# Kernel optimization log

Measured on AMD Instinct MI355X. Metric: run time of the kernel, lower is better.

The kernel has to match this reference:

```python
import jax, jax.numpy as jnp
import numpy as np

B, D, H, S = 32768, 512, 8, 3  # batch, stream_dim, heads, num_streams
DH = D // H
EPS = 1e-5


def setup_inputs() -> dict:
    key = jax.random.key(0)
    ks = jax.random.split(key, 16)
    sc = lambda fan_in: 1.0 / np.sqrt(fan_in)
    return {
        "kinematic_h": jax.random.normal(ks[0], (B, D), jnp.float32),
        "color_h": jax.random.normal(ks[1], (B, D), jnp.float32),
        "spinor_h": jax.random.normal(ks[2], (B, D), jnp.float32),
        # MultiheadAttention packed in-proj and out-proj
        "w_in": jax.random.normal(ks[3], (3 * D, D), jnp.float32) * sc(D),
        "b_in": jnp.zeros((3 * D,), jnp.float32),
        "w_out": jax.random.normal(ks[4], (D, D), jnp.float32) * sc(D),
        "b_out": jnp.zeros((D,), jnp.float32),
        # stream gate: Linear(3D -> 3) + softmax
        "w_gate": jax.random.normal(ks[5], (S, S * D), jnp.float32) * sc(S * D),
        "b_gate": jnp.zeros((S,), jnp.float32),
        # fusion MLP: Linear(3D -> 2D), SiLU, Linear(2D -> D)
        "w1": jax.random.normal(ks[6], (2 * D, S * D), jnp.float32) * sc(S * D),
        "b1": jnp.zeros((2 * D,), jnp.float32),
        "w2": jax.random.normal(ks[7], (D, 2 * D), jnp.float32) * sc(2 * D),
        "b2": jnp.zeros((D,), jnp.float32),
        # LayerNorm
        "gamma": jnp.ones((D,), jnp.float32),
        "beta": jnp.zeros((D,), jnp.float32),
    }


def reference(kinematic_h, color_h, spinor_h, w_in, b_in, w_out, b_out,
              w_gate, b_gate, w1, b1, w2, b2, gamma, beta):
    stacked = jnp.stack([kinematic_h, color_h, spinor_h], axis=1)  # [B,S,D]
    b = stacked.shape[0]
    # self-attention (Q=K=V=stacked), packed QKV projection
    qkv = stacked @ w_in.T + b_in  # [B,S,3D]
    q, k, v = jnp.split(qkv, 3, axis=-1)
    q = q.reshape(b, S, H, DH)
    k = k.reshape(b, S, H, DH)
    v = v.reshape(b, S, H, DH)
    scores = jnp.einsum("bqhd,bkhd->bhqk", q, k) / np.sqrt(DH)
    attn = jax.nn.softmax(scores, axis=-1)
    out = jnp.einsum("bhqk,bkhd->bqhd", attn, v).reshape(b, S, D)
    attn_out = stacked + (out @ w_out.T + b_out)  # residual, [B,S,D]
    # gating softmax over streams
    flat = attn_out.reshape(b, S * D)
    gates = jax.nn.softmax(flat @ w_gate.T + b_gate, axis=-1)[..., None]  # [B,S,1]
    gated = (attn_out * gates).reshape(b, S * D)
    # fusion MLP (dropout=eval no-op)
    h = jax.nn.silu(gated @ w1.T + b1)
    fused = h @ w2.T + b2  # [B,D]
    # LayerNorm
    mu = jnp.mean(fused, axis=-1, keepdims=True)
    var = jnp.var(fused, axis=-1, keepdims=True)
    return (fused - mu) * jax.lax.rsqrt(var + EPS) * gamma + beta
```

## Files before the change

kernel.cpp:

```cpp
#include <hip/hip_runtime.h>
#include <hip/hip_bf16.h>
#include <stdint.h>


typedef float f32x4 __attribute__((ext_vector_type(4)));
typedef short bf16x8 __attribute__((ext_vector_type(8)));

__device__ __forceinline__ float bf2f(unsigned short h) {
  return __uint_as_float(((unsigned)h) << 16);
}
__device__ __forceinline__ unsigned short f2bf(float f) {
  __hip_bfloat16 h = __float2bfloat16(f);
  return *reinterpret_cast<unsigned short*>(&h);
}
__device__ __forceinline__ unsigned pack2bf(float lo, float hi) {
  __hip_bfloat162 h2 = __float22bfloat162_rn(make_float2(lo, hi));
  return *reinterpret_cast<unsigned*>(&h2);
}
__device__ __forceinline__ uint2 f2bf4p(float4 v) {
  return make_uint2(pack2bf(v.x, v.y), pack2bf(v.z, v.w));
}

__device__ __forceinline__ void async_cp16(const void* g, void* lds) {
  __builtin_amdgcn_global_load_lds(
      (const __attribute__((address_space(1))) void*)g,
      (__attribute__((address_space(3))) void*)lds, 16, 0, 0);
}

__global__ void __launch_bounds__(256) cvtbf(const float4* __restrict__ src,
                                             uint2* __restrict__ dst, int n4) {
  int i = blockIdx.x * 256 + threadIdx.x;
  if (i < n4) dst[i] = f2bf4p(src[i]);
}

__global__ void __launch_bounds__(256) pack3(const float4* __restrict__ X0,
                                             const float4* __restrict__ X1,
                                             const float4* __restrict__ X2,
                                             uint2* __restrict__ S) {
  int tid = blockIdx.x * 256 + threadIdx.x;
  int b = tid >> 7, c = tid & 127;
  long base = (long)(3 * b) * 128 + c;
  S[base]       = f2bf4p(X0[tid]);
  S[base + 128] = f2bf4p(X1[tid]);
  S[base + 256] = f2bf4p(X2[tid]);
}

__global__ void __launch_bounds__(256)
qkv_attn(const unsigned short* __restrict__ S,
         const unsigned short* __restrict__ Wi,
         const float* __restrict__ bin,
         unsigned short* __restrict__ AO) {
  __shared__ unsigned short lds[96 * 200];
  unsigned short* Abuf = lds;
  unsigned short* Bbuf = lds + 6144;

  const int t = threadIdx.x;
  const int lane = t & 63;
  const int wave = t >> 6;
  const int wm = wave >> 1, wn = wave & 1;

  const int ny = gridDim.y;
  const int id = blockIdx.y * 8 + blockIdx.x;
  const int xcd = id & 7, j = id >> 3;
  const int h = j & 7;
  const long m0 = (long)(xcd * (ny >> 3) + (j >> 3)) * 96;

  const int trow = t >> 3;
  const int swz = ((t & 7) ^ (trow & 7)) << 3;
  const unsigned short* Ag = S + (m0 + trow) * 512 + swz;
  const unsigned short* Bg = Wi + ((long)h * 64 + trow) * 512 + swz;
  unsigned short* AsD = Abuf + t * 8;
  unsigned short* BsD = Bbuf + t * 8;

  f32x4 acc[3][6] = {};
  const int arow0 = wm * 48 + (lane & 15);
  const int brow0 = wn * 96 + (lane & 15);

  for (int k0 = 0; k0 < 512; k0 += 64) {
    __syncthreads();
#pragma unroll
    for (int r = 0; r < 3; r++)
      async_cp16(Ag + (long)r * 32 * 512 + k0, AsD + r * 2048);
#pragma unroll
    for (int r = 0; r < 6; r++)
      async_cp16(Bg + (long)((r >> 1) * 512 + (r & 1) * 32) * 512 + k0, BsD + r * 2048);
    __syncthreads();
#pragma unroll
    for (int kk = 0; kk < 2; kk++) {
      const int sc = ((kk * 4 + (lane >> 4)) ^ (lane & 7)) << 3;
      bf16x8 af[3], bfr[6];
#pragma unroll
      for (int mt = 0; mt < 3; mt++)
        af[mt] = *(const bf16x8*)&Abuf[(arow0 + mt * 16) * 64 + sc];
#pragma unroll
      for (int nt = 0; nt < 6; nt++)
        bfr[nt] = *(const bf16x8*)&Bbuf[(brow0 + nt * 16) * 64 + sc];
#pragma unroll
      for (int mt = 0; mt < 3; mt++)
#pragma unroll
        for (int nt = 0; nt < 6; nt++)
          acc[mt][nt] = __builtin_amdgcn_mfma_f32_16x16x32_bf16(
              af[mt], bfr[nt], acc[mt][nt], 0, 0, 0);
    }
  }

  __syncthreads();
  const int crow0 = wm * 48 + ((lane >> 4) << 2);
  const int ccol0 = wn * 96 + (lane & 15);
#pragma unroll
  for (int nt = 0; nt < 6; nt++) {
    const int col = ccol0 + nt * 16;
    const float bv = bin[(col >> 6) * 512 + h * 64 + (col & 63)];
#pragma unroll
    for (int mt = 0; mt < 3; mt++) {
      const int rb = (crow0 + mt * 16) * 200 + col;
      const unsigned p01 = pack2bf(acc[mt][nt][0] + bv, acc[mt][nt][1] + bv);
      const unsigned p23 = pack2bf(acc[mt][nt][2] + bv, acc[mt][nt][3] + bv);
      lds[rb]       = (unsigned short)p01;
      lds[rb + 200] = (unsigned short)(p01 >> 16);
      lds[rb + 400] = (unsigned short)p23;
      lds[rb + 600] = (unsigned short)(p23 >> 16);
    }
  }
  __syncthreads();

  const int bi = lane >> 3;
  const int l8 = lane & 7;
  const int r0 = (wave * 8 + bi) * 3;
  float q[3][8], k[3][8], v[3][8];
#pragma unroll
  for (int s = 0; s < 3; s++) {
    const unsigned short* rowp = &lds[(r0 + s) * 200 + l8 * 8];
    uint4 qu = *(const uint4*)(rowp);
    uint4 ku = *(const uint4*)(rowp + 64);
    uint4 vu = *(const uint4*)(rowp + 128);
    const unsigned* qw = (const unsigned*)&qu;
    const unsigned* kw = (const unsigned*)&ku;
    const unsigned* vw = (const unsigned*)&vu;
#pragma unroll
    for (int jj = 0; jj < 4; jj++) {
      q[s][2 * jj]     = __uint_as_float(qw[jj] << 16);
      q[s][2 * jj + 1] = __uint_as_float(qw[jj] & 0xffff0000u);
      k[s][2 * jj]     = __uint_as_float(kw[jj] << 16);
      k[s][2 * jj + 1] = __uint_as_float(kw[jj] & 0xffff0000u);
      v[s][2 * jj]     = __uint_as_float(vw[jj] << 16);
      v[s][2 * jj + 1] = __uint_as_float(vw[jj] & 0xffff0000u);
    }
  }
  float p[3][3];
#pragma unroll
  for (int s = 0; s < 3; s++)
#pragma unroll
    for (int u = 0; u < 3; u++) {
      float d = 0.f;
#pragma unroll
      for (int e = 0; e < 8; e++) d = fmaf(q[s][e], k[u][e], d);
      p[s][u] = d;
    }
#pragma unroll
  for (int m = 1; m < 8; m <<= 1)
#pragma unroll
    for (int s = 0; s < 3; s++)
#pragma unroll
      for (int u = 0; u < 3; u++) p[s][u] += __shfl_xor(p[s][u], m, 64);

  unsigned short* ob = AO + (m0 + r0) * 512 + h * 64 + l8 * 8;
#pragma unroll
  for (int s = 0; s < 3; s++) {
    float a0 = p[s][0] * 0.125f, a1 = p[s][1] * 0.125f, a2 = p[s][2] * 0.125f;
    float mx = fmaxf(a0, fmaxf(a1, a2));
    float e0 = __expf(a0 - mx), e1 = __expf(a1 - mx), e2 = __expf(a2 - mx);
    float inv = 1.0f / (e0 + e1 + e2);
    unsigned ow[4];
#pragma unroll
    for (int jj = 0; jj < 4; jj++) {
      float lo = (e0 * v[0][2 * jj] + e1 * v[1][2 * jj] + e2 * v[2][2 * jj]) * inv;
      float hi = (e0 * v[0][2 * jj + 1] + e1 * v[1][2 * jj + 1] + e2 * v[2][2 * jj + 1]) * inv;
      ow[jj] = pack2bf(lo, hi);
    }
    *(uint4*)(ob + s * 512) = *(uint4*)ow;
  }
}

enum { EPI_BF16 = 0, EPI_RES = 1, EPI_SILU = 2, EPI_F32 = 3 };

template <int EPI>
__global__ void __launch_bounds__(256)
gemm_bt(const unsigned short* __restrict__ A,
        const unsigned short* __restrict__ W,
        const float* __restrict__ bias,
        const unsigned short* __restrict__ Res,
        void* __restrict__ Out,
        int K, int N) {
  __shared__ unsigned short As[128 * 64];
  __shared__ unsigned short Bs[128 * 64];
  const int t = threadIdx.x;
  const int lane = t & 63;
  const int wave = t >> 6;
  const int wm = wave >> 1, wn = wave & 1;

  const int nb = gridDim.x;
  const int nblocks = nb * gridDim.y;
  const int id = blockIdx.y * nb + blockIdx.x;
  const int lid = ((nblocks & 7) == 0) ? ((id & 7) * (nblocks >> 3) + (id >> 3)) : id;
  const long bm = (long)(lid / nb) * 128;
  const long bn = (long)(lid % nb) * 128;

  const int srow = t >> 3;
  const int schunk = ((t & 7) ^ (srow & 7)) << 3;
  const unsigned short* Ag = A + (bm + srow) * (long)K + schunk;
  const unsigned short* Wg = W + (bn + srow) * (long)K + schunk;
  unsigned short* AsD = As + t * 8;
  unsigned short* BsD = Bs + t * 8;

  f32x4 acc[4][4] = {};
  const int arow0 = wm * 64 + (lane & 15);
  const int brow0 = wn * 64 + (lane & 15);

  for (int k0 = 0; k0 < K; k0 += 64) {
    __syncthreads();
#pragma unroll
    for (int i = 0; i < 4; i++) {
      async_cp16(Ag + (long)(i * 32) * K + k0, AsD + i * 2048);
      async_cp16(Wg + (long)(i * 32) * K + k0, BsD + i * 2048);
    }
    __syncthreads();
#pragma unroll
    for (int kk = 0; kk < 2; kk++) {
      const int sc = ((kk * 4 + (lane >> 4)) ^ (lane & 7)) << 3;
      bf16x8 af[4], bfr[4];
#pragma unroll
      for (int mt = 0; mt < 4; mt++)
        af[mt] = *(const bf16x8*)&As[(arow0 + mt * 16) * 64 + sc];
#pragma unroll
      for (int nt = 0; nt < 4; nt++)
        bfr[nt] = *(const bf16x8*)&Bs[(brow0 + nt * 16) * 64 + sc];
#pragma unroll
      for (int mt = 0; mt < 4; mt++)
#pragma unroll
        for (int nt = 0; nt < 4; nt++)
          acc[mt][nt] = __builtin_amdgcn_mfma_f32_16x16x32_bf16(
              af[mt], bfr[nt], acc[mt][nt], 0, 0, 0);
    }
  }

  const long row0 = bm + wm * 64 + ((lane >> 4) << 2);
  const int col0 = (int)bn + wn * 64 + (lane & 15);
#pragma unroll
  for (int nt = 0; nt < 4; nt++) {
    const int col = col0 + nt * 16;
    const float bv = bias[col];
#pragma unroll
    for (int mt = 0; mt < 4; mt++) {
      const long rbase = row0 + mt * 16;
#pragma unroll
      for (int r = 0; r < 4; r++) {
        float v = acc[mt][nt][r] + bv;
        const long idx = (rbase + r) * (long)N + col;
        if (EPI == EPI_RES) v += bf2f(Res[idx]);
        if (EPI == EPI_SILU) v = v * (1.0f / (1.0f + __expf(-v)));
        if (EPI == EPI_F32)
          ((float*)Out)[idx] = v;
        else
          ((unsigned short*)Out)[idx] = f2bf(v);
      }
    }
  }
}

__global__ void __launch_bounds__(256) gate3(const unsigned short* AT,
                                             const float* __restrict__ WG,
                                             const float* __restrict__ BG,
                                             unsigned short* G) {
  int row = blockIdx.x * 4 + (threadIdx.x >> 6);
  int lane = threadIdx.x & 63;
  const unsigned short* rp = AT + (long)row * 1536 + lane * 8;
  float x[3][8];
  float p[3] = {0.f, 0.f, 0.f};
#pragma unroll
  for (int seg = 0; seg < 3; seg++) {
    uint4 u = *(const uint4*)(rp + seg * 512);
    const unsigned* uw = (const unsigned*)&u;
#pragma unroll
    for (int j = 0; j < 4; j++) {
      x[seg][2 * j]     = __uint_as_float(uw[j] << 16);
      x[seg][2 * j + 1] = __uint_as_float(uw[j] & 0xffff0000u);
    }
    const int e0 = seg * 512 + lane * 8;
#pragma unroll
    for (int g = 0; g < 3; g++) {
      const float* wp = WG + g * 1536 + e0;
#pragma unroll
      for (int e = 0; e < 8; e++) p[g] = fmaf(x[seg][e], wp[e], p[g]);
    }
  }
#pragma unroll
  for (int m = 1; m < 64; m <<= 1)
#pragma unroll
    for (int g = 0; g < 3; g++) p[g] += __shfl_xor(p[g], m, 64);
  float g0 = p[0] + BG[0], g1 = p[1] + BG[1], g2 = p[2] + BG[2];
  float mx = fmaxf(g0, fmaxf(g1, g2));
  g0 = __expf(g0 - mx); g1 = __expf(g1 - mx); g2 = __expf(g2 - mx);
  float inv = 1.0f / (g0 + g1 + g2);
  float gs[3] = {g0 * inv, g1 * inv, g2 * inv};
  unsigned short* op = G + (long)row * 1536 + lane * 8;
#pragma unroll
  for (int seg = 0; seg < 3; seg++) {
    unsigned ow[4];
#pragma unroll
    for (int j = 0; j < 4; j++)
      ow[j] = pack2bf(x[seg][2 * j] * gs[seg], x[seg][2 * j + 1] * gs[seg]);
    *(uint4*)(op + seg * 512) = *(uint4*)ow;
  }
}

__global__ void __launch_bounds__(256) lnorm(const float* __restrict__ F,
                                             const float* __restrict__ gamma,
                                             const float* __restrict__ beta,
                                             float* __restrict__ out) {
  int row = blockIdx.x * 4 + (threadIdx.x >> 6);
  int lane = threadIdx.x & 63;
  const float4* fr = (const float4*)(F + (long)row * 512);
  float4 a = fr[lane], c = fr[lane + 64];
  float s = a.x + a.y + a.z + a.w + c.x + c.y + c.z + c.w;
  float ss = a.x * a.x + a.y * a.y + a.z * a.z + a.w * a.w +
             c.x * c.x + c.y * c.y + c.z * c.z + c.w * c.w;
#pragma unroll
  for (int m = 1; m < 64; m <<= 1) {
    s += __shfl_xor(s, m, 64);
    ss += __shfl_xor(ss, m, 64);
  }
  float mean = s * (1.0f / 512.0f);
  float var = ss * (1.0f / 512.0f) - mean * mean;
  float rstd = rsqrtf(var + 1e-5f);
  const float4* g4 = (const float4*)gamma;
  const float4* b4 = (const float4*)beta;
  float4 g0 = g4[lane], g1 = g4[lane + 64], be0 = b4[lane], be1 = b4[lane + 64];
  float4 o0, o1;
  o0.x = (a.x - mean) * rstd * g0.x + be0.x;
  o0.y = (a.y - mean) * rstd * g0.y + be0.y;
  o0.z = (a.z - mean) * rstd * g0.z + be0.z;
  o0.w = (a.w - mean) * rstd * g0.w + be0.w;
  o1.x = (c.x - mean) * rstd * g1.x + be1.x;
  o1.y = (c.y - mean) * rstd * g1.y + be1.y;
  o1.z = (c.z - mean) * rstd * g1.z + be1.z;
  o1.w = (c.w - mean) * rstd * g1.w + be1.w;
  float4* orow = (float4*)(out + (long)row * 512);
  orow[lane] = o0;
  orow[lane + 64] = o1;
}

extern "C" void kernel_launch(void* const* d_in, const int* in_sizes, int n_in,
                              void* d_out, int out_size, void* d_ws, size_t ws_size,
                              hipStream_t stream) {
  const float* kin    = (const float*)d_in[0];
  const float* colr   = (const float*)d_in[1];
  const float* spi    = (const float*)d_in[2];
  const float* w_in   = (const float*)d_in[3];
  const float* b_in   = (const float*)d_in[4];
  const float* w_out  = (const float*)d_in[5];
  const float* b_out  = (const float*)d_in[6];
  const float* w_gate = (const float*)d_in[7];
  const float* b_gate = (const float*)d_in[8];
  const float* w1     = (const float*)d_in[9];
  const float* b1     = (const float*)d_in[10];
  const float* w2     = (const float*)d_in[11];
  const float* b2     = (const float*)d_in[12];
  const float* gamma  = (const float*)d_in[13];
  const float* beta   = (const float*)d_in[14];
  float* out = (float*)d_out;

  long Bc = 32768;
  while (Bc > 1024 && (size_t)(6291456 + 9216 * Bc) > ws_size) Bc >>= 1;
  const int nch = (int)(32768 / Bc);

  char* ws = (char*)d_ws;
  unsigned short* Wic = (unsigned short*)(ws);
  unsigned short* Woc = (unsigned short*)(ws + 1572864);
  unsigned short* W1c = (unsigned short*)(ws + 2097152);
  unsigned short* W2c = (unsigned short*)(ws + 5242880);
  char* Sb  = ws + 6291456;
  char* AOb = Sb + 3072 * Bc;
  char* ATb = AOb + 3072 * Bc;

  cvtbf<<<768, 256, 0, stream>>>((const float4*)w_in, (uint2*)Wic, 196608);
  cvtbf<<<256, 256, 0, stream>>>((const float4*)w_out, (uint2*)Woc, 65536);
  cvtbf<<<1536, 256, 0, stream>>>((const float4*)w1, (uint2*)W1c, 393216);
  cvtbf<<<512, 256, 0, stream>>>((const float4*)w2, (uint2*)W2c, 131072);

  for (int c = 0; c < nch; c++) {
    const long boff = (long)c * Bc;
    unsigned short* S_c  = (unsigned short*)Sb;
    unsigned short* AO_c = (unsigned short*)AOb;
    unsigned short* AT_c = (unsigned short*)ATb;
    unsigned short* G_c  = AT_c;
    unsigned short* H_c  = (unsigned short*)AOb;
    float*          F_c  = (float*)Sb;

    pack3<<<(int)(Bc / 2), 256, 0, stream>>>(
        (const float4*)(kin + boff * 512), (const float4*)(colr + boff * 512),
        (const float4*)(spi + boff * 512), (uint2*)S_c);
    qkv_attn<<<dim3(8, (int)(Bc / 32)), 256, 0, stream>>>(S_c, Wic, b_in, AO_c);
    gemm_bt<EPI_RES><<<dim3(4, (int)(3 * Bc / 128)), 256, 0, stream>>>(
        AO_c, Woc, b_out, S_c, AT_c, 512, 512);
    gate3<<<(int)(Bc / 4), 256, 0, stream>>>(AT_c, w_gate, b_gate, G_c);
    gemm_bt<EPI_SILU><<<dim3(8, (int)(Bc / 128)), 256, 0, stream>>>(
        G_c, W1c, b1, nullptr, H_c, 1536, 1024);
    gemm_bt<EPI_F32><<<dim3(4, (int)(Bc / 128)), 256, 0, stream>>>(
        H_c, W2c, b2, nullptr, F_c, 1024, 512);
    lnorm<<<(int)(Bc / 4), 256, 0, stream>>>(F_c, gamma, beta, out + boff * 512);
  }
}
```

Measured before the change: 777.9 us.

## Fuse input packing into QKV kernel and merge weight conversions into one launch

Removes the separate pack3 kernel. The QKV/attention kernel now loads the fp32 stream inputs directly, converts them to bf16 in registers, and writes them into LDS, prefetching the next K-slice into registers during the MFMA work. Blocks with head 0 also write the packed bf16 stream buffer that the later residual GEMM needs. The four weight-conversion launches become one kernel, and launch bounds now request 4 blocks per SM. The cost is double-width fp32 A reads repeated across the 8 head blocks in place of async bf16 copies, plus higher register pressure.

```diff
diff --git a/kernel.cpp b/kernel.cpp
--- a/kernel.cpp
+++ b/kernel.cpp
@@ -27,28 +27,28 @@
       (__attribute__((address_space(3))) void*)lds, 16, 0, 0);
 }
 
-__global__ void __launch_bounds__(256) cvtbf(const float4* __restrict__ src,
-                                             uint2* __restrict__ dst, int n4) {
+__global__ void __launch_bounds__(256) cvtall(const float4* __restrict__ w_in,
+                                              const float4* __restrict__ w_out,
+                                              const float4* __restrict__ w1,
+                                              const float4* __restrict__ w2,
+                                              uint2* __restrict__ dst) {
   int i = blockIdx.x * 256 + threadIdx.x;
-  if (i < n4) dst[i] = f2bf4p(src[i]);
-}
-
-__global__ void __launch_bounds__(256) pack3(const float4* __restrict__ X0,
-                                             const float4* __restrict__ X1,
-                                             const float4* __restrict__ X2,
-                                             uint2* __restrict__ S) {
-  int tid = blockIdx.x * 256 + threadIdx.x;
-  int b = tid >> 7, c = tid & 127;
-  long base = (long)(3 * b) * 128 + c;
-  S[base]       = f2bf4p(X0[tid]);
-  S[base + 128] = f2bf4p(X1[tid]);
-  S[base + 256] = f2bf4p(X2[tid]);
-}
-
-__global__ void __launch_bounds__(256)
-qkv_attn(const unsigned short* __restrict__ S,
+  const float4* s;
+  int off;
+  if (i < 196608)      { s = w_in;  off = 0; }
+  else if (i < 262144) { s = w_out; off = 196608; }
+  else if (i < 655360) { s = w1;    off = 262144; }
+  else                 { s = w2;    off = 655360; }
+  dst[i] = f2bf4p(s[i - off]);
+}
+
+__global__ void __launch_bounds__(256, 4)
+qkv_attn(const float* __restrict__ X0,
+         const float* __restrict__ X1,
+         const float* __restrict__ X2,
          const unsigned short* __restrict__ Wi,
          const float* __restrict__ bin,
+         unsigned short* __restrict__ Sout,
          unsigned short* __restrict__ AO) {
   __shared__ unsigned short lds[96 * 200];
   unsigned short* Abuf = lds;
@@ -67,7 +67,18 @@
 
   const int trow = t >> 3;
   const int swz = ((t & 7) ^ (trow & 7)) << 3;
-  const unsigned short* Ag = S + (m0 + trow) * 512 + swz;
+  const long b0 = m0 / 3;
+  const float* Aptr[3];
+  unsigned short* Sptr[3];
+#pragma unroll
+  for (int r = 0; r < 3; r++) {
+    const int rl = trow + 32 * r;
+    const int br = rl / 3;
+    const int sr = rl - 3 * br;
+    const float* X = (sr == 0) ? X0 : (sr == 1) ? X1 : X2;
+    Aptr[r] = X + (b0 + br) * 512 + swz;
+    Sptr[r] = Sout + (m0 + rl) * 512 + swz;
+  }
   const unsigned short* Bg = Wi + ((long)h * 64 + trow) * 512 + swz;
   unsigned short* AsD = Abuf + t * 8;
   unsigned short* BsD = Bbuf + t * 8;
@@ -76,15 +87,34 @@
   const int arow0 = wm * 48 + (lane & 15);
   const int brow0 = wn * 96 + (lane & 15);
 
+  float4 Alo[3], Ahi[3];
+#pragma unroll
+  for (int r = 0; r < 3; r++) {
+    Alo[r] = *(const float4*)(Aptr[r]);
+    Ahi[r] = *(const float4*)(Aptr[r] + 4);
+  }
+
   for (int k0 = 0; k0 < 512; k0 += 64) {
     __syncthreads();
 #pragma unroll
-    for (int r = 0; r < 3; r++)
-      async_cp16(Ag + (long)r * 32 * 512 + k0, AsD + r * 2048);
+    for (int r = 0; r < 3; r++) {
+      const uint4 uv = make_uint4(
+          pack2bf(Alo[r].x, Alo[r].y), pack2bf(Alo[r].z, Alo[r].w),
+          pack2bf(Ahi[r].x, Ahi[r].y), pack2bf(Ahi[r].z, Ahi[r].w));
+      *(uint4*)(AsD + r * 2048) = uv;
+      if (h == 0) *(uint4*)(Sptr[r] + k0) = uv;
+    }
 #pragma unroll
     for (int r = 0; r < 6; r++)
       async_cp16(Bg + (long)((r >> 1) * 512 + (r & 1) * 32) * 512 + k0, BsD + r * 2048);
     __syncthreads();
+    if (k0 + 64 < 512) {
+#pragma unroll
+      for (int r = 0; r < 3; r++) {
+        Alo[r] = *(const float4*)(Aptr[r] + k0 + 64);
+        Ahi[r] = *(const float4*)(Aptr[r] + k0 + 68);
+      }
+    }
 #pragma unroll
     for (int kk = 0; kk < 2; kk++) {
       const int sc = ((kk * 4 + (lane >> 4)) ^ (lane & 7)) << 3;
@@ -383,10 +413,9 @@
   char* AOb = Sb + 3072 * Bc;
   char* ATb = AOb + 3072 * Bc;
 
-  cvtbf<<<768, 256, 0, stream>>>((const float4*)w_in, (uint2*)Wic, 196608);
-  cvtbf<<<256, 256, 0, stream>>>((const float4*)w_out, (uint2*)Woc, 65536);
-  cvtbf<<<1536, 256, 0, stream>>>((const float4*)w1, (uint2*)W1c, 393216);
-  cvtbf<<<512, 256, 0, stream>>>((const float4*)w2, (uint2*)W2c, 131072);
+  cvtall<<<3072, 256, 0, stream>>>((const float4*)w_in, (const float4*)w_out,
+                                   (const float4*)w1, (const float4*)w2,
+                                   (uint2*)ws);
 
   for (int c = 0; c < nch; c++) {
     const long boff = (long)c * Bc;
@@ -397,10 +426,9 @@
     unsigned short* H_c  = (unsigned short*)AOb;
     float*          F_c  = (float*)Sb;
 
-    pack3<<<(int)(Bc / 2), 256, 0, stream>>>(
-        (const float4*)(kin + boff * 512), (const float4*)(colr + boff * 512),
-        (const float4*)(spi + boff * 512), (uint2*)S_c);
-    qkv_attn<<<dim3(8, (int)(Bc / 32)), 256, 0, stream>>>(S_c, Wic, b_in, AO_c);
+    qkv_attn<<<dim3(8, (int)(Bc / 32)), 256, 0, stream>>>(
+        kin + boff * 512, colr + boff * 512, spi + boff * 512,
+        Wic, b_in, S_c, AO_c);
     gemm_bt<EPI_RES><<<dim3(4, (int)(3 * Bc / 128)), 256, 0, stream>>>(
         AO_c, Woc, b_out, S_c, AT_c, 512, 512);
     gate3<<<(int)(Bc / 4), 256, 0, stream>>>(AT_c, w_gate, b_gate, G_c);
```

After: 1.187 ms. 1.53x slower.
